# Kernel optimization log

Hardware: AMD Instinct MI355X
Metric: run time of the kernel (lower is better)

Reference implementation:

```python
import jax, jax.numpy as jnp
import numpy as np

N = 50000      # nodes
E = 800000     # edges
IN = 128       # in_channels
HID = 128      # hidden_channels
OUT = 2        # out_channels (edge classes)
HEADS = 8      # EGConv default num_heads
BASES = 4      # EGConv default num_bases
FH = HID // HEADS  # per-head feature dim = 16


def _egconv(x, Wb, Wc, bc, b, row, col, norm, n):
    """One EGConv layer (aggregators=['symnorm']), self-loops already in row/col/norm.
    Wb: [in, BASES*FH] basis projection (no bias).
    Wc: [in, HEADS*BASES], bc: combination weights linear.
    b : [HID] output bias.
    """
    bases = x @ Wb                                            # [n, BASES*FH]
    msg = bases[row] * norm[:, None]                          # gather + symnorm scale
    agg = jax.ops.segment_sum(msg, col, num_segments=n)       # scatter-add -> [n, BASES*FH]
    w = (x @ Wc + bc).reshape(n, HEADS, BASES)                # per-node combination weights
    out = jnp.einsum('nhb,nbf->nhf', w, agg.reshape(n, BASES, FH))
    return out.reshape(n, HEADS * FH) + b


def setup_inputs() -> dict:
    key = jax.random.key(0)
    ks = jax.random.split(key, 12)
    s = 0.05
    inp = {
        'x': jax.random.normal(ks[0], (N, IN), jnp.float32),
        'edge_index': jax.random.randint(ks[1], (2, E), 0, N, jnp.int64),
        # conv1
        'Wb1': jax.random.normal(ks[2], (IN, BASES * FH), jnp.float32) * s,
        'Wc1': jax.random.normal(ks[3], (IN, HEADS * BASES), jnp.float32) * s,
        'bc1': jnp.zeros((HEADS * BASES,), jnp.float32),
        'b1': jnp.zeros((HID,), jnp.float32),
        # conv2
        'Wb2': jax.random.normal(ks[4], (HID, BASES * FH), jnp.float32) * s,
        'Wc2': jax.random.normal(ks[5], (HID, HEADS * BASES), jnp.float32) * s,
        'bc2': jnp.zeros((HEADS * BASES,), jnp.float32),
        'b2': jnp.zeros((HID,), jnp.float32),
        # edge classifier
        'Wcls': jax.random.normal(ks[6], (2 * HID, OUT), jnp.float32) * s,
        'bcls': jnp.zeros((OUT,), jnp.float32),
    }
    return inp


def reference(x, edge_index, Wb1, Wc1, bc1, b1, Wb2, Wc2, bc2, b2, Wcls, bcls):
    n = x.shape[0]
    # add self loops (EGConv default add_self_loops=True) + gcn_norm symnorm weights
    sl = jnp.arange(n, dtype=edge_index.dtype)
    row = jnp.concatenate([edge_index[0], sl])
    col = jnp.concatenate([edge_index[1], sl])
    deg = jax.ops.segment_sum(jnp.ones(row.shape[0], x.dtype), col, num_segments=n)
    dis = jnp.where(deg > 0, deg, 1.0) ** -0.5
    dis = jnp.where(deg > 0, dis, 0.0)
    norm = dis[row] * dis[col]                                # symnorm edge weight

    h = jax.nn.relu(_egconv(x, Wb1, Wc1, bc1, b1, row, col, norm, n))
    h = _egconv(h, Wb2, Wc2, bc2, b2, row, col, norm, n)

    # edge classifier: gather endpoint embeddings of ORIGINAL edges, concat, linear
    e = jnp.concatenate([h[edge_index[0]], h[edge_index[1]]], axis=-1)  # [E, 2*HID]
    return e @ Wcls + bcls
```

## Files before the change

kernel.cpp:

```cpp
#include <hip/hip_runtime.h>
#include <hip/hip_fp16.h>

#define NN 50000
#define EE 800000
#define NB_E2 1563
#define NWIN 8
#define WIN 6250
#define EPB 1024
#define NCHUNK 782
#define NFILL (NCHUNK * 8)
#define NGX 196

__global__ void k_count(const int* __restrict__ ei, int* cnt, int* __restrict__ rank) {
    int t = blockIdx.x * 256 + threadIdx.x;
    if (t < EE / 2) {
        int2 cc = *(const int2*)(ei + EE + 2 * t);
        int r0 = atomicAdd(&cnt[cc.x], 1);
        int r1 = atomicAdd(&cnt[cc.y], 1);
        *(int2*)(rank + 2 * t) = make_int2(r0, r1);
    }
}

__global__ void k_scan1(const int* __restrict__ cnt, int* sloc, int* bsum,
                        float* dis, int n) {
    __shared__ int s[256];
    int tid = threadIdx.x;
    int i = blockIdx.x * 256 + tid;
    int v = (i < n) ? cnt[i] : 0;
    if (i < n) dis[i] = rsqrtf((float)v + 1.0f);
    s[tid] = v;
    __syncthreads();
    for (int off = 1; off < 256; off <<= 1) {
        int t2 = 0;
        if (tid >= off) t2 = s[tid - off];
        __syncthreads();
        if (tid >= off) s[tid] += t2;
        __syncthreads();
    }
    if (i < n) sloc[i] = s[tid] - v;
    if (tid == 255) bsum[blockIdx.x] = s[255];
}

__global__ void k_scan23(const int* __restrict__ sloc, const int* __restrict__ bsum,
                         const int* __restrict__ cnt, int2* sd, int* starts,
                         int n, int nb) {
    __shared__ int sb[256];
    int tid = threadIdx.x, b = blockIdx.x;
    int v = (tid < nb && tid < b) ? bsum[tid] : 0;
    sb[tid] = v;
    __syncthreads();
    for (int off = 128; off; off >>= 1) {
        if (tid < off) sb[tid] += sb[tid + off];
        __syncthreads();
    }
    int boff = sb[0];
    int i = b * 256 + tid;
    if (i < n) {
        int st = sloc[i] + boff;
        sd[i] = make_int2(st, cnt[i]);
        starts[i] = st;
    }
}

__device__ __forceinline__ void gemm_body(
    int bx, int grp, int tid, float* xt,
    const float* __restrict__ x, const float* __restrict__ Wb,
    const float* __restrict__ Wc, const float* __restrict__ bc,
    const float* __restrict__ dis,
    __half* __restrict__ bsh, float* __restrict__ wcomb, int n)
{
    int row0 = bx * 256;
    int row = row0 + tid;
    bool valid = row < n;

    const float* W = (grp < 2) ? (Wb + grp * 32) : Wc;
    const int ldw = (grp < 2) ? 64 : 32;

    float acc[32];
#pragma unroll
    for (int c = 0; c < 32; c++) acc[c] = 0.f;

    for (int s = 0; s < 4; s++) {
        int base_k = s * 32;
        float4 v[8];
#pragma unroll
        for (int i = 0; i < 8; i++) {
            int idx = i * 256 + tid;
            int r = idx >> 3;
            int k4 = idx & 7;
            int gr = row0 + r;
            v[i] = (gr < n) ? *(const float4*)(x + (size_t)gr * 128 + base_k + k4 * 4)
                            : make_float4(0.f, 0.f, 0.f, 0.f);
        }
        __syncthreads();
#pragma unroll
        for (int i = 0; i < 8; i++) {
            int idx = i * 256 + tid;
            int r = idx >> 3;
            int k4 = idx & 7;
            xt[(k4 * 4 + 0) * 257 + r] = v[i].x;
            xt[(k4 * 4 + 1) * 257 + r] = v[i].y;
            xt[(k4 * 4 + 2) * 257 + r] = v[i].z;
            xt[(k4 * 4 + 3) * 257 + r] = v[i].w;
        }
        __syncthreads();

        const float* Ws = W + base_k * ldw;
#pragma unroll 8
        for (int k = 0; k < 32; k++) {
            float xs = xt[k * 257 + tid];
            const float* wk = Ws + k * ldw;
#pragma unroll
            for (int c = 0; c < 32; c++) acc[c] = fmaf(xs, wk[c], acc[c]);
        }
    }

    if (!valid) return;
    if (grp < 2) {
        float d = dis[row];
        __half2 hh[16];
#pragma unroll
        for (int c = 0; c < 16; c++)
            hh[c] = __floats2half2_rn(acc[2 * c] * d, acc[2 * c + 1] * d);
        uint4* bo = (uint4*)(bsh + (size_t)row * 64 + grp * 32);
        const uint4* src = (const uint4*)hh;
#pragma unroll
        for (int c = 0; c < 4; c++) bo[c] = src[c];
    } else {
        float4* wo = (float4*)(wcomb + (size_t)row * 32);
#pragma unroll
        for (int c = 0; c < 8; c++)
            wo[c] = make_float4(acc[4*c] + bc[4*c], acc[4*c+1] + bc[4*c+1],
                                acc[4*c+2] + bc[4*c+2], acc[4*c+3] + bc[4*c+3]);
    }
}

__global__ __launch_bounds__(256) void k_fill_gemm(
    const int* __restrict__ ei, const int* __restrict__ rank,
    const int* __restrict__ starts, int* __restrict__ csr,
    const float* __restrict__ x, const float* __restrict__ Wb,
    const float* __restrict__ Wc, const float* __restrict__ bc,
    const float* __restrict__ dis,
    __half* __restrict__ bsh, float* __restrict__ wcomb, int n)
{
    __shared__ float xt[32 * 257];
    int b = blockIdx.x;
    if (b < NFILL) {
        int w = b & 7;
        int chunk = b >> 3;
        int base = chunk * EPB + threadIdx.x * 4;
        int lo = w * WIN, hi = lo + WIN;
        if (base + 3 < EE) {
            int4 rr = *(const int4*)(ei + base);
            int4 cc = *(const int4*)(ei + EE + base);
            int4 rk = *(const int4*)(rank + base);
            if (cc.x >= lo && cc.x < hi) csr[starts[cc.x] + rk.x] = rr.x;
            if (cc.y >= lo && cc.y < hi) csr[starts[cc.y] + rk.y] = rr.y;
            if (cc.z >= lo && cc.z < hi) csr[starts[cc.z] + rk.z] = rr.z;
            if (cc.w >= lo && cc.w < hi) csr[starts[cc.w] + rk.w] = rr.w;
        } else {
            for (int e = 0; e < 4; e++) {
                int t = base + e;
                if (t < EE) {
                    int c = ei[EE + t];
                    if (c >= lo && c < hi) csr[starts[c] + rank[t]] = ei[t];
                }
            }
        }
        return;
    }
    int bb = b - NFILL;
    int grp = bb / NGX;
    int bx = bb - grp * NGX;
    gemm_body(bx, grp, threadIdx.x, xt, x, Wb, Wc, bc, dis, bsh, wcomb, n);
}

__global__ __launch_bounds__(256) void k_gemm(
    const float* __restrict__ x, const float* __restrict__ Wb,
    const float* __restrict__ Wc, const float* __restrict__ bc,
    const float* __restrict__ dis,
    __half* __restrict__ bsh, float* __restrict__ wcomb, int n)
{
    __shared__ float xt[32 * 257];
    gemm_body(blockIdx.x, blockIdx.y, threadIdx.x, xt, x, Wb, Wc, bc, dis,
              bsh, wcomb, n);
}

__device__ __forceinline__ void h8_to_f8(uint4 v, float* f) {
    float2 a = __half22float2(*(const __half2*)&v.x);
    float2 b = __half22float2(*(const __half2*)&v.y);
    float2 c = __half22float2(*(const __half2*)&v.z);
    float2 d = __half22float2(*(const __half2*)&v.w);
    f[0] = a.x; f[1] = a.y; f[2] = b.x; f[3] = b.y;
    f[4] = c.x; f[5] = c.y; f[6] = d.x; f[7] = d.y;
}

template<int LAYER2>
__global__ __launch_bounds__(256) void k_agg(
    const int* __restrict__ csr, const int2* __restrict__ sd,
    const __half* __restrict__ bsh, const float* __restrict__ dis,
    const float* __restrict__ wcomb, const float* __restrict__ bias,
    float* __restrict__ h,
    const float* __restrict__ Wcls, const float* __restrict__ bcls,
    float* __restrict__ p, int n)
{
    int wid = (blockIdx.x * 256 + threadIdx.x) >> 6;
    int lane = threadIdx.x & 63;
    if (wid >= n) return;
    int2 s2 = sd[wid];
    int start = s2.x, deg = s2.y;
    int g = lane >> 3, q = lane & 7;
    const uint4* bsp4 = (const uint4*)bsh;

    float acc[8];
#pragma unroll
    for (int j = 0; j < 8; j++) acc[j] = 0.f;

    int nw = (deg + 63) >> 6;
    for (int wdw = 0; wdw < nw; wdw++) {
        int wb = wdw << 6;
        int rem = min(deg - wb, 64);
        int idxv = (lane < rem) ? csr[start + wb + lane] : 0;
        int e0 = 0;
        for (; e0 + 16 <= rem; e0 += 16) {
            int r0 = __shfl(idxv, e0 + g, 64);
            int r1 = __shfl(idxv, e0 + 8 + g, 64);
            uint4 v0 = bsp4[(size_t)r0 * 8 + q];
            uint4 v1 = bsp4[(size_t)r1 * 8 + q];
            float f0[8], f1[8];
            h8_to_f8(v0, f0);
            h8_to_f8(v1, f1);
#pragma unroll
            for (int j = 0; j < 8; j++) acc[j] += f0[j] + f1[j];
        }
        for (; e0 < rem; e0 += 8) {
            int r = __shfl(idxv, e0 + g, 64);
            float m = (e0 + g < rem) ? 1.f : 0.f;
            uint4 v = bsp4[(size_t)r * 8 + q];
            float f[8];
            h8_to_f8(v, f);
#pragma unroll
            for (int j = 0; j < 8; j++) acc[j] = fmaf(f[j], m, acc[j]);
        }
    }

#pragma unroll
    for (int off = 8; off <= 32; off <<= 1)
#pragma unroll
        for (int j = 0; j < 8; j++) acc[j] += __shfl_xor(acc[j], off, 64);

    uint4 sv = bsp4[(size_t)wid * 8 + q];
    float sf[8];
    h8_to_f8(sv, sf);
    float d = dis[wid];
#pragma unroll
    for (int j = 0; j < 8; j++) acc[j] = (acc[j] + sf[j]) * d;

    int srcq = lane >> 3;
    float v0 = __shfl(acc[0], srcq, 64);
    float v1 = __shfl(acc[1], srcq, 64);
    float v2 = __shfl(acc[2], srcq, 64);
    float v3 = __shfl(acc[3], srcq, 64);
    float v4 = __shfl(acc[4], srcq, 64);
    float v5 = __shfl(acc[5], srcq, 64);
    float v6 = __shfl(acc[6], srcq, 64);
    float v7 = __shfl(acc[7], srcq, 64);
    int jj = lane & 7;
    float a = (jj == 0) ? v0 : (jj == 1) ? v1 : (jj == 2) ? v2 : (jj == 3) ? v3
            : (jj == 4) ? v4 : (jj == 5) ? v5 : (jj == 6) ? v6 : v7;

    int fh = lane & 15;
    float a0 = __shfl(a, fh, 64);
    float a1 = __shfl(a, 16 + fh, 64);
    float a2 = __shfl(a, 32 + fh, 64);
    float a3 = __shfl(a, 48 + fh, 64);
    const float* wn = wcomb + (size_t)wid * 32;
    int hd = lane >> 4;
    float s1 = bias[lane];
    float s2v = bias[64 + lane];
    s1 = fmaf(wn[hd * 4 + 0], a0, s1);
    s1 = fmaf(wn[hd * 4 + 1], a1, s1);
    s1 = fmaf(wn[hd * 4 + 2], a2, s1);
    s1 = fmaf(wn[hd * 4 + 3], a3, s1);
    s2v = fmaf(wn[(4 + hd) * 4 + 0], a0, s2v);
    s2v = fmaf(wn[(4 + hd) * 4 + 1], a1, s2v);
    s2v = fmaf(wn[(4 + hd) * 4 + 2], a2, s2v);
    s2v = fmaf(wn[(4 + hd) * 4 + 3], a3, s2v);

    if (!LAYER2) {
        s1 = fmaxf(s1, 0.f);
        s2v = fmaxf(s2v, 0.f);
        h[(size_t)wid * 128 + lane] = s1;
        h[(size_t)wid * 128 + 64 + lane] = s2v;
    } else {
        float r0 = s1 * Wcls[lane * 2 + 0] + s2v * Wcls[(64 + lane) * 2 + 0];
        float r1 = s1 * Wcls[lane * 2 + 1] + s2v * Wcls[(64 + lane) * 2 + 1];
        float r2 = s1 * Wcls[(128 + lane) * 2 + 0] + s2v * Wcls[(192 + lane) * 2 + 0];
        float r3 = s1 * Wcls[(128 + lane) * 2 + 1] + s2v * Wcls[(192 + lane) * 2 + 1];
#pragma unroll
        for (int off = 32; off; off >>= 1) {
            r0 += __shfl_xor(r0, off, 64);
            r1 += __shfl_xor(r1, off, 64);
            r2 += __shfl_xor(r2, off, 64);
            r3 += __shfl_xor(r3, off, 64);
        }
        if (lane == 0) {
            p[wid * 4 + 0] = r0 + bcls[0];
            p[wid * 4 + 1] = r1 + bcls[1];
            p[wid * 4 + 2] = r2;
            p[wid * 4 + 3] = r3;
        }
    }
}

__global__ void k_edge(const int* __restrict__ ei, const float* __restrict__ p,
                       float* __restrict__ out)
{
    int t = blockIdx.x * blockDim.x + threadIdx.x;
    if (t >= EE / 2) return;
    int2 rr = *(const int2*)(ei + 2 * t);
    int2 cc = *(const int2*)(ei + EE + 2 * t);
    float2 pt0 = *(const float2*)(p + rr.x * 4);
    float2 pt1 = *(const float2*)(p + rr.y * 4);
    float2 pb0 = *(const float2*)(p + cc.x * 4 + 2);
    float2 pb1 = *(const float2*)(p + cc.y * 4 + 2);
    float4 o;
    o.x = pt0.x + pb0.x;
    o.y = pt0.y + pb0.y;
    o.z = pt1.x + pb1.x;
    o.w = pt1.y + pb1.y;
    *(float4*)(out + (size_t)t * 4) = o;
}

extern "C" void kernel_launch(void* const* d_in, const int* in_sizes, int n_in,
                              void* d_out, int out_size, void* d_ws, size_t ws_size,
                              hipStream_t stream) {
    const float* x    = (const float*)d_in[0];
    const int*   ei   = (const int*)d_in[1];
    const float* Wb1  = (const float*)d_in[2];
    const float* Wc1  = (const float*)d_in[3];
    const float* bc1  = (const float*)d_in[4];
    const float* b1   = (const float*)d_in[5];
    const float* Wb2  = (const float*)d_in[6];
    const float* Wc2  = (const float*)d_in[7];
    const float* bc2  = (const float*)d_in[8];
    const float* b2   = (const float*)d_in[9];
    const float* Wcls = (const float*)d_in[10];
    const float* bcls = (const float*)d_in[11];
    float* out = (float*)d_out;

    char* ws = (char*)d_ws;
    size_t off = 0;
    auto alloc = [&](size_t bytes) {
        void* pp = ws + off;
        off += (bytes + 15) & ~(size_t)15;
        return pp;
    };

    float*  dis    = (float*)alloc(50048 * 4);
    __half* bsh    = (__half*)alloc((size_t)NN * 64 * 2);
    float*  wcomb  = (float*)alloc((size_t)NN * 32 * 4);
    float*  h      = (float*)alloc((size_t)NN * 128 * 4);
    float*  p      = (float*)alloc((size_t)NN * 4 * 4);
    int*    cnt    = (int*)alloc(50048 * 4);
    int*    sloc   = (int*)alloc(50048 * 4);
    int*    starts = (int*)alloc(50048 * 4);
    int*    bsum   = (int*)alloc(256 * 4);
    int2*   sd     = (int2*)alloc((size_t)50048 * 8);
    int*    csr    = (int*)alloc((size_t)EE * 4);
    int*    rank   = (int*)alloc((size_t)EE * 4);

    const int B = 256;
    int gN   = (NN + B - 1) / B;
    int gN64 = (NN * 64) / B;
    dim3 gG(NGX, 3);

    hipMemsetAsync(cnt, 0, NN * sizeof(int), stream);
    k_count<<<NB_E2, B, 0, stream>>>(ei, cnt, rank);
    k_scan1<<<gN, B, 0, stream>>>(cnt, sloc, bsum, dis, NN);
    k_scan23<<<gN, B, 0, stream>>>(sloc, bsum, cnt, sd, starts, NN, gN);

    k_fill_gemm<<<NFILL + NGX * 3, B, 0, stream>>>(
        ei, rank, starts, csr, x, Wb1, Wc1, bc1, dis, bsh, wcomb, NN);
    k_agg<0><<<gN64, B, 0, stream>>>(csr, sd, bsh, dis, wcomb, b1, h,
                                     Wcls, bcls, p, NN);

    k_gemm<<<gG, B, 0, stream>>>(h, Wb2, Wc2, bc2, dis, bsh, wcomb, NN);
    k_agg<1><<<gN64, B, 0, stream>>>(csr, sd, bsh, dis, wcomb, b2, h,
                                     Wcls, bcls, p, NN);

    k_edge<<<NB_E2, B, 0, stream>>>(ei, p, out);
}
```

Before: 282.0 us.

## Fuse all stages into one persistent cooperative kernel with grid syncs

Replaces the memset and eight separate launches with a single cooperative persistent kernel. Each stage runs as a grid-stride loop over work units, separated by grid.sync barriers. The GEMM k-tile shrinks from 32 to 16 so its shared-memory tile fits alongside the higher occupancy target set by launch_bounds(256,6). This removes per-launch overhead and tail gaps between stages, but adds grid-wide barrier cost and may lower per-stage efficiency through register limits and the smaller GEMM tile.

```diff
diff --git a/kernel.cpp b/kernel.cpp
--- a/kernel.cpp
+++ b/kernel.cpp
@@ -1,78 +1,32 @@
 #include <hip/hip_runtime.h>
 #include <hip/hip_fp16.h>
+#include <hip/hip_cooperative_groups.h>
+
+namespace cg = cooperative_groups;
 
 #define NN 50000
 #define EE 800000
-#define NB_E2 1563
 #define NWIN 8
 #define WIN 6250
 #define EPB 1024
 #define NCHUNK 782
 #define NFILL (NCHUNK * 8)
 #define NGX 196
-
-__global__ void k_count(const int* __restrict__ ei, int* cnt, int* __restrict__ rank) {
-    int t = blockIdx.x * 256 + threadIdx.x;
-    if (t < EE / 2) {
-        int2 cc = *(const int2*)(ei + EE + 2 * t);
-        int r0 = atomicAdd(&cnt[cc.x], 1);
-        int r1 = atomicAdd(&cnt[cc.y], 1);
-        *(int2*)(rank + 2 * t) = make_int2(r0, r1);
-    }
-}
-
-__global__ void k_scan1(const int* __restrict__ cnt, int* sloc, int* bsum,
-                        float* dis, int n) {
-    __shared__ int s[256];
-    int tid = threadIdx.x;
-    int i = blockIdx.x * 256 + tid;
-    int v = (i < n) ? cnt[i] : 0;
-    if (i < n) dis[i] = rsqrtf((float)v + 1.0f);
-    s[tid] = v;
-    __syncthreads();
-    for (int off = 1; off < 256; off <<= 1) {
-        int t2 = 0;
-        if (tid >= off) t2 = s[tid - off];
-        __syncthreads();
-        if (tid >= off) s[tid] += t2;
-        __syncthreads();
-    }
-    if (i < n) sloc[i] = s[tid] - v;
-    if (tid == 255) bsum[blockIdx.x] = s[255];
-}
-
-__global__ void k_scan23(const int* __restrict__ sloc, const int* __restrict__ bsum,
-                         const int* __restrict__ cnt, int2* sd, int* starts,
-                         int n, int nb) {
-    __shared__ int sb[256];
-    int tid = threadIdx.x, b = blockIdx.x;
-    int v = (tid < nb && tid < b) ? bsum[tid] : 0;
-    sb[tid] = v;
-    __syncthreads();
-    for (int off = 128; off; off >>= 1) {
-        if (tid < off) sb[tid] += sb[tid + off];
-        __syncthreads();
-    }
-    int boff = sb[0];
-    int i = b * 256 + tid;
-    if (i < n) {
-        int st = sloc[i] + boff;
-        sd[i] = make_int2(st, cnt[i]);
-        starts[i] = st;
-    }
-}
-
-__device__ __forceinline__ void gemm_body(
+#define NGEMM (NGX * 3)
+#define NU_SCAN 196
+#define NU_E2 1563
+#define NU_AGG 12500
+
+__device__ __forceinline__ void gemm_unit(
     int bx, int grp, int tid, float* xt,
-    const float* __restrict__ x, const float* __restrict__ Wb,
+    const float* __restrict__ xsrc, const float* __restrict__ Wb,
     const float* __restrict__ Wc, const float* __restrict__ bc,
     const float* __restrict__ dis,
-    __half* __restrict__ bsh, float* __restrict__ wcomb, int n)
+    __half* __restrict__ bsh, float* __restrict__ wcomb)
 {
     int row0 = bx * 256;
     int row = row0 + tid;
-    bool valid = row < n;
-
+    bool valid = row < NN;
     const float* W = (grp < 2) ? (Wb + grp * 32) : Wc;
     const int ldw = (grp < 2) ? 64 : 32;
 
@@ -80,40 +34,40 @@
 #pragma unroll
     for (int c = 0; c < 32; c++) acc[c] = 0.f;
 
-    for (int s = 0; s < 4; s++) {
-        int base_k = s * 32;
-        float4 v[8];
-#pragma unroll
-        for (int i = 0; i < 8; i++) {
+    for (int s = 0; s < 8; s++) {
+        int base_k = s * 16;
+        float4 v[4];
+#pragma unroll
+        for (int i = 0; i < 4; i++) {
             int idx = i * 256 + tid;
-            int r = idx >> 3;
-            int k4 = idx & 7;
+            int r = idx >> 2;
+            int k4 = idx & 3;
             int gr = row0 + r;
-            v[i] = (gr < n) ? *(const float4*)(x + (size_t)gr * 128 + base_k + k4 * 4)
-                            : make_float4(0.f, 0.f, 0.f, 0.f);
-        }
-        __syncthreads();
-#pragma unroll
-        for (int i = 0; i < 8; i++) {
+            v[i] = (gr < NN) ? *(const float4*)(xsrc + (size_t)gr * 128 + base_k + k4 * 4)
+                             : make_float4(0.f, 0.f, 0.f, 0.f);
+        }
+        __syncthreads();
+#pragma unroll
+        for (int i = 0; i < 4; i++) {
             int idx = i * 256 + tid;
-            int r = idx >> 3;
-            int k4 = idx & 7;
+            int r = idx >> 2;
+            int k4 = idx & 3;
             xt[(k4 * 4 + 0) * 257 + r] = v[i].x;
             xt[(k4 * 4 + 1) * 257 + r] = v[i].y;
             xt[(k4 * 4 + 2) * 257 + r] = v[i].z;
             xt[(k4 * 4 + 3) * 257 + r] = v[i].w;
         }
         __syncthreads();
-
         const float* Ws = W + base_k * ldw;
 #pragma unroll 8
-        for (int k = 0; k < 32; k++) {
+        for (int k = 0; k < 16; k++) {
             float xs = xt[k * 257 + tid];
             const float* wk = Ws + k * ldw;
 #pragma unroll
             for (int c = 0; c < 32; c++) acc[c] = fmaf(xs, wk[c], acc[c]);
         }
     }
+    __syncthreads();
 
     if (!valid) return;
     if (grp < 2) {
@@ -133,57 +87,6 @@
             wo[c] = make_float4(acc[4*c] + bc[4*c], acc[4*c+1] + bc[4*c+1],
                                 acc[4*c+2] + bc[4*c+2], acc[4*c+3] + bc[4*c+3]);
     }
-}
-
-__global__ __launch_bounds__(256) void k_fill_gemm(
-    const int* __restrict__ ei, const int* __restrict__ rank,
-    const int* __restrict__ starts, int* __restrict__ csr,
-    const float* __restrict__ x, const float* __restrict__ Wb,
-    const float* __restrict__ Wc, const float* __restrict__ bc,
-    const float* __restrict__ dis,
-    __half* __restrict__ bsh, float* __restrict__ wcomb, int n)
-{
-    __shared__ float xt[32 * 257];
-    int b = blockIdx.x;
-    if (b < NFILL) {
-        int w = b & 7;
-        int chunk = b >> 3;
-        int base = chunk * EPB + threadIdx.x * 4;
-        int lo = w * WIN, hi = lo + WIN;
-        if (base + 3 < EE) {
-            int4 rr = *(const int4*)(ei + base);
-            int4 cc = *(const int4*)(ei + EE + base);
-            int4 rk = *(const int4*)(rank + base);
-            if (cc.x >= lo && cc.x < hi) csr[starts[cc.x] + rk.x] = rr.x;
-            if (cc.y >= lo && cc.y < hi) csr[starts[cc.y] + rk.y] = rr.y;
-            if (cc.z >= lo && cc.z < hi) csr[starts[cc.z] + rk.z] = rr.z;
-            if (cc.w >= lo && cc.w < hi) csr[starts[cc.w] + rk.w] = rr.w;
-        } else {
-            for (int e = 0; e < 4; e++) {
-                int t = base + e;
-                if (t < EE) {
-                    int c = ei[EE + t];
-                    if (c >= lo && c < hi) csr[starts[c] + rank[t]] = ei[t];
-                }
-            }
-        }
-        return;
-    }
-    int bb = b - NFILL;
-    int grp = bb / NGX;
-    int bx = bb - grp * NGX;
-    gemm_body(bx, grp, threadIdx.x, xt, x, Wb, Wc, bc, dis, bsh, wcomb, n);
-}
-
-__global__ __launch_bounds__(256) void k_gemm(
-    const float* __restrict__ x, const float* __restrict__ Wb,
-    const float* __restrict__ Wc, const float* __restrict__ bc,
-    const float* __restrict__ dis,
-    __half* __restrict__ bsh, float* __restrict__ wcomb, int n)
-{
-    __shared__ float xt[32 * 257];
-    gemm_body(blockIdx.x, blockIdx.y, threadIdx.x, xt, x, Wb, Wc, bc, dis,
-              bsh, wcomb, n);
 }
 
 __device__ __forceinline__ void h8_to_f8(uint4 v, float* f) {
@@ -196,17 +99,15 @@
 }
 
 template<int LAYER2>
-__global__ __launch_bounds__(256) void k_agg(
+__device__ __forceinline__ void agg_node(
+    int wid, int lane,
     const int* __restrict__ csr, const int2* __restrict__ sd,
     const __half* __restrict__ bsh, const float* __restrict__ dis,
     const float* __restrict__ wcomb, const float* __restrict__ bias,
     float* __restrict__ h,
     const float* __restrict__ Wcls, const float* __restrict__ bcls,
-    float* __restrict__ p, int n)
+    float* __restrict__ p)
 {
-    int wid = (blockIdx.x * 256 + threadIdx.x) >> 6;
-    int lane = threadIdx.x & 63;
-    if (wid >= n) return;
     int2 s2 = sd[wid];
     int start = s2.x, deg = s2.y;
     int g = lane >> 3, q = lane & 7;
@@ -313,30 +214,154 @@
     }
 }
 
-__global__ void k_edge(const int* __restrict__ ei, const float* __restrict__ p,
-                       float* __restrict__ out)
+__global__ __launch_bounds__(256, 6) void k_mega(
+    const int* __restrict__ ei, const float* __restrict__ x,
+    const float* __restrict__ Wb1, const float* __restrict__ Wc1,
+    const float* __restrict__ bc1, const float* __restrict__ b1,
+    const float* __restrict__ Wb2, const float* __restrict__ Wc2,
+    const float* __restrict__ bc2, const float* __restrict__ b2,
+    const float* __restrict__ Wcls, const float* __restrict__ bcls,
+    float* __restrict__ out,
+    int* cnt, int* rank, int* sloc, int* bsum, int* starts,
+    int2* sd, float* dis, int* csr, __half* bsh, float* wcomb,
+    float* h, float* p)
 {
-    int t = blockIdx.x * blockDim.x + threadIdx.x;
-    if (t >= EE / 2) return;
-    int2 rr = *(const int2*)(ei + 2 * t);
-    int2 cc = *(const int2*)(ei + EE + 2 * t);
-    float2 pt0 = *(const float2*)(p + rr.x * 4);
-    float2 pt1 = *(const float2*)(p + rr.y * 4);
-    float2 pb0 = *(const float2*)(p + cc.x * 4 + 2);
-    float2 pb1 = *(const float2*)(p + cc.y * 4 + 2);
-    float4 o;
-    o.x = pt0.x + pb0.x;
-    o.y = pt0.y + pb0.y;
-    o.z = pt1.x + pb1.x;
-    o.w = pt1.y + pb1.y;
-    *(float4*)(out + (size_t)t * 4) = o;
+    __shared__ float smem[16 * 257];
+    int* si = (int*)smem;
+    cg::grid_group grid = cg::this_grid();
+    const int G = gridDim.x;
+    const int tid = threadIdx.x;
+
+    for (int u = blockIdx.x; u < NU_SCAN; u += G) {
+        int i = u * 256 + tid;
+        if (i < NN) cnt[i] = 0;
+    }
+    grid.sync();
+
+    for (int u = blockIdx.x; u < NU_E2; u += G) {
+        int t = u * 256 + tid;
+        if (t < EE / 2) {
+            int2 cc = *(const int2*)(ei + EE + 2 * t);
+            int r0 = atomicAdd(&cnt[cc.x], 1);
+            int r1 = atomicAdd(&cnt[cc.y], 1);
+            *(int2*)(rank + 2 * t) = make_int2(r0, r1);
+        }
+    }
+    grid.sync();
+
+    for (int u = blockIdx.x; u < NU_SCAN; u += G) {
+        int i = u * 256 + tid;
+        int v = (i < NN) ? cnt[i] : 0;
+        if (i < NN) dis[i] = rsqrtf((float)v + 1.0f);
+        si[tid] = v;
+        __syncthreads();
+        for (int off = 1; off < 256; off <<= 1) {
+            int t2 = 0;
+            if (tid >= off) t2 = si[tid - off];
+            __syncthreads();
+            if (tid >= off) si[tid] += t2;
+            __syncthreads();
+        }
+        if (i < NN) sloc[i] = si[tid] - v;
+        if (tid == 255) bsum[u] = si[255];
+        __syncthreads();
+    }
+    grid.sync();
+
+    for (int u = blockIdx.x; u < NU_SCAN; u += G) {
+        int v = (tid < NU_SCAN && tid < u) ? bsum[tid] : 0;
+        si[tid] = v;
+        __syncthreads();
+        for (int off = 128; off; off >>= 1) {
+            if (tid < off) si[tid] += si[tid + off];
+            __syncthreads();
+        }
+        int boff = si[0];
+        __syncthreads();
+        int i = u * 256 + tid;
+        if (i < NN) {
+            int st = sloc[i] + boff;
+            sd[i] = make_int2(st, cnt[i]);
+            starts[i] = st;
+        }
+    }
+    grid.sync();
+
+    for (int u = blockIdx.x; u < NFILL + NGEMM; u += G) {
+        if (u < NFILL) {
+            int w = u & 7;
+            int chunk = u >> 3;
+            int base = chunk * EPB + tid * 4;
+            int lo = w * WIN, hi = lo + WIN;
+            if (base + 3 < EE) {
+                int4 rr = *(const int4*)(ei + base);
+                int4 cc = *(const int4*)(ei + EE + base);
+                int4 rk = *(const int4*)(rank + base);
+                if (cc.x >= lo && cc.x < hi) csr[starts[cc.x] + rk.x] = rr.x;
+                if (cc.y >= lo && cc.y < hi) csr[starts[cc.y] + rk.y] = rr.y;
+                if (cc.z >= lo && cc.z < hi) csr[starts[cc.z] + rk.z] = rr.z;
+                if (cc.w >= lo && cc.w < hi) csr[starts[cc.w] + rk.w] = rr.w;
+            } else {
+                for (int e = 0; e < 4; e++) {
+                    int t = base + e;
+                    if (t < EE) {
+                        int c = ei[EE + t];
+                        if (c >= lo && c < hi) csr[starts[c] + rank[t]] = ei[t];
+                    }
+                }
+            }
+        } else {
+            int gu = u - NFILL;
+            int grp = gu / NGX;
+            int bx = gu - grp * NGX;
+            gemm_unit(bx, grp, tid, smem, x, Wb1, Wc1, bc1, dis, bsh, wcomb);
+        }
+    }
+    grid.sync();
+
+    for (int u = blockIdx.x; u < NU_AGG; u += G) {
+        int wid = u * 4 + (tid >> 6);
+        agg_node<0>(wid, tid & 63, csr, sd, bsh, dis, wcomb, b1, h, Wcls, bcls, p);
+    }
+    grid.sync();
+
+    for (int u = blockIdx.x; u < NGEMM; u += G) {
+        int grp = u / NGX;
+        int bx = u - grp * NGX;
+        gemm_unit(bx, grp, tid, smem, h, Wb2, Wc2, bc2, dis, bsh, wcomb);
+    }
+    grid.sync();
+
+    for (int u = blockIdx.x; u < NU_AGG; u += G) {
+        int wid = u * 4 + (tid >> 6);
+        agg_node<1>(wid, tid & 63, csr, sd, bsh, dis, wcomb, b2, h, Wcls, bcls, p);
+    }
+    grid.sync();
+
+    for (int u = blockIdx.x; u < NU_E2; u += G) {
+        int t = u * 256 + tid;
+        if (t < EE / 2) {
+            int2 rr = *(const int2*)(ei + 2 * t);
+            int2 cc = *(const int2*)(ei + EE + 2 * t);
+            float2 pt0 = *(const float2*)(p + rr.x * 4);
+            float2 pt1 = *(const float2*)(p + rr.y * 4);
+            float2 pb0 = *(const float2*)(p + cc.x * 4 + 2);
+            float2 pb1 = *(const float2*)(p + cc.y * 4 + 2);
+            float4 o;
+            o.x = pt0.x + pb0.x;
+            o.y = pt0.y + pb0.y;
+            o.z = pt1.x + pb1.x;
+            o.w = pt1.y + pb1.y;
+            *(float4*)(out + (size_t)t * 4) = o;
+        }
+    }
 }
 
 extern "C" void kernel_launch(void* const* d_in, const int* in_sizes, int n_in,
                               void* d_out, int out_size, void* d_ws, size_t ws_size,
                               hipStream_t stream) {
+    const int*   ei   = (const int*)d_in[1];
     const float* x    = (const float*)d_in[0];
-    const int*   ei   = (const int*)d_in[1];
     const float* Wb1  = (const float*)d_in[2];
     const float* Wc1  = (const float*)d_in[3];
     const float* bc1  = (const float*)d_in[4];
@@ -370,24 +395,19 @@
     int*    csr    = (int*)alloc((size_t)EE * 4);
     int*    rank   = (int*)alloc((size_t)EE * 4);
 
-    const int B = 256;
-    int gN   = (NN + B - 1) / B;
-    int gN64 = (NN * 64) / B;
-    dim3 gG(NGX, 3);
-
-    hipMemsetAsync(cnt, 0, NN * sizeof(int), stream);
-    k_count<<<NB_E2, B, 0, stream>>>(ei, cnt, rank);
-    k_scan1<<<gN, B, 0, stream>>>(cnt, sloc, bsum, dis, NN);
-    k_scan23<<<gN, B, 0, stream>>>(sloc, bsum, cnt, sd, starts, NN, gN);
-
-    k_fill_gemm<<<NFILL + NGX * 3, B, 0, stream>>>(
-        ei, rank, starts, csr, x, Wb1, Wc1, bc1, dis, bsh, wcomb, NN);
-    k_agg<0><<<gN64, B, 0, stream>>>(csr, sd, bsh, dis, wcomb, b1, h,
-                                     Wcls, bcls, p, NN);
-
-    k_gemm<<<gG, B, 0, stream>>>(h, Wb2, Wc2, bc2, dis, bsh, wcomb, NN);
-    k_agg<1><<<gN64, B, 0, stream>>>(csr, sd, bsh, dis, wcomb, b2, h,
-                                     Wcls, bcls, p, NN);
-
-    k_edge<<<NB_E2, B, 0, stream>>>(ei, p, out);
+    int nb = 0;
+    if (hipOccupancyMaxActiveBlocksPerMultiprocessor(&nb, (const void*)k_mega, 256, 0)
+            != hipSuccess || nb <= 0)
+        nb = 4;
+    if (nb > 8) nb = 8;
+    int G = nb * 256;
+
+    void* args[] = {
+        (void*)&ei, (void*)&x, (void*)&Wb1, (void*)&Wc1, (void*)&bc1, (void*)&b1,
+        (void*)&Wb2, (void*)&Wc2, (void*)&bc2, (void*)&b2, (void*)&Wcls, (void*)&bcls,
+        (void*)&out, (void*)&cnt, (void*)&rank, (void*)&sloc, (void*)&bsum,
+        (void*)&starts, (void*)&sd, (void*)&dis, (void*)&csr, (void*)&bsh,
+        (void*)&wcomb, (void*)&h, (void*)&p
+    };
+    hipLaunchCooperativeKernel((void*)k_mega, dim3(G), dim3(256), args, 0, stream);
 }
```

Result: slower. 1.046 ms (+271.0%).
